# Optimization experiments

Measured on AMD Instinct MI355X. Metric: run time of the kernel, lower is better.

## Reference

```python
import jax, jax.numpy as jnp
import numpy as np

EMBED_DIM = 768
NUM_HEADS = 12
HEAD_DIM = EMBED_DIM // NUM_HEADS


def setup_inputs() -> dict:
    key = jax.random.key(0)
    ks = jax.random.split(key, 9)
    d = EMBED_DIM
    s = 1.0 / np.sqrt(d)
    x = jax.random.normal(ks[0], (1, 4096, d), dtype=jnp.float32)
    # nn.Linear weights stored as [out, in]; init ~ U(-1/sqrt(in), 1/sqrt(in))
    wq = jax.random.uniform(ks[1], (d, d), jnp.float32, -s, s)
    bq = jax.random.uniform(ks[2], (d,), jnp.float32, -s, s)
    wk = jax.random.uniform(ks[3], (d, d), jnp.float32, -s, s)
    bk = jax.random.uniform(ks[4], (d,), jnp.float32, -s, s)
    wv = jax.random.uniform(ks[5], (d, d), jnp.float32, -s, s)
    bv = jax.random.uniform(ks[6], (d,), jnp.float32, -s, s)
    ww = jax.random.uniform(ks[7], (d, d), jnp.float32, -s, s)
    bw = jax.random.uniform(ks[8], (d,), jnp.float32, -s, s)
    return {"x": x, "wq": wq, "bq": bq, "wk": wk, "bk": bk,
            "wv": wv, "bv": bv, "ww": ww, "bw": bw}


def reference(x, wq, bq, wk, bk, wv, bv, ww, bw):
    B, S, D = x.shape
    H, Hd = NUM_HEADS, HEAD_DIM
    # Linear: x @ W^T + b, then split heads -> [B, H, S, Hd]
    def proj(w, b):
        y = x @ w.T + b
        return y.reshape(B, S, H, Hd).transpose(0, 2, 1, 3)
    q = proj(wq, bq)
    k = proj(wk, bk)
    v = proj(wv, bv)
    scores = jnp.einsum('bhqd,bhkd->bhqk', q, k) / jnp.sqrt(jnp.float32(Hd))
    attn = jax.nn.softmax(scores, axis=-1)
    out = jnp.einsum('bhqk,bhkd->bhqd', attn, v)  # [B,H,S,Hd]
    out = out.transpose(0, 2, 1, 3).reshape(B, S, D)
    return out @ ww.T + bw
```

## Files before the change

kernel.cpp:

```cpp
#include <hip/hip_runtime.h>
#include <cstdio>


using u16 = unsigned short;
typedef __bf16 bf16x8 __attribute__((ext_vector_type(8)));
typedef float f32x4 __attribute__((ext_vector_type(4)));
typedef float f32x16 __attribute__((ext_vector_type(16)));
typedef unsigned int u32x4 __attribute__((ext_vector_type(4)));
typedef u16 u16x4 __attribute__((ext_vector_type(4)));

constexpr int SEQ = 4096;
constexpr int DIM = 768;
constexpr int NH = 12;
constexpr int HD = 64;
constexpr int LDT = 72;
constexpr int LDA2 = 40;
constexpr int LDM = 68;
constexpr float SM_PRE = 0.18033688011112042f;
constexpr float DEFER_THR = 8.0f;

__device__ __forceinline__ u16 f2bf(float f) {
  union { float f; unsigned u; } v{f};
  unsigned r = v.u + 0x7fffu + ((v.u >> 16) & 1u);
  return (u16)(r >> 16);
}
__device__ __forceinline__ unsigned cvtpk_bf16(float a, float b) {
  unsigned r;
  asm("v_cvt_pk_bf16_f32 %0, %1, %2" : "=v"(r) : "v"(a), "v"(b));
  return r;
}
__device__ __forceinline__ void swap32(unsigned& a, unsigned& b) {
  asm volatile("v_permlane32_swap_b32 %0, %1" : "+v"(a), "+v"(b));
}
__device__ __forceinline__ bf16x8 bc16(const u16* p) {
  return __builtin_bit_cast(bf16x8, *(const u32x4*)p);
}
__device__ __forceinline__ float fmax3(float a, float b, float c) {
  return fmaxf(fmaxf(a, b), c);
}

__global__ __launch_bounds__(256) void prep_all(const float* __restrict__ x,
                                                const float* __restrict__ wq,
                                                const float* __restrict__ wk,
                                                const float* __restrict__ wv,
                                                u16* __restrict__ xb,
                                                u16* __restrict__ wqb,
                                                u16* __restrict__ wkb,
                                                u16* __restrict__ wvb) {
  constexpr size_t NX = (size_t)SEQ * DIM, NW = (size_t)DIM * DIM;
  size_t i = ((size_t)blockIdx.x * 256 + threadIdx.x) * 8;
  const float* src;
  u16* dst;
  size_t off;
  if (i < NX) { src = x; dst = xb; off = i; }
  else if (i < NX + NW) { src = wq; dst = wqb; off = i - NX; }
  else if (i < NX + 2 * NW) { src = wk; dst = wkb; off = i - NX - 2 * NW + NW; }
  else { src = wv; dst = wvb; off = i - NX - 3 * NW + NW; }
  float4 f0 = *(const float4*)(src + off);
  float4 f1 = *(const float4*)(src + off + 4);
  u32x4 w = {cvtpk_bf16(f0.x, f0.y), cvtpk_bf16(f0.z, f0.w),
             cvtpk_bf16(f1.x, f1.y), cvtpk_bf16(f1.z, f1.w)};
  *(u32x4*)(dst + off) = w;
}

__global__ __launch_bounds__(256) void prep_one(const float* __restrict__ w,
                                                u16* __restrict__ wb) {
  size_t off = ((size_t)blockIdx.x * 256 + threadIdx.x) * 8;
  float4 f0 = *(const float4*)(w + off);
  float4 f1 = *(const float4*)(w + off + 4);
  u32x4 v = {cvtpk_bf16(f0.x, f0.y), cvtpk_bf16(f0.z, f0.w),
             cvtpk_bf16(f1.x, f1.y), cvtpk_bf16(f1.z, f1.w)};
  *(u32x4*)(wb + off) = v;
}

__global__ __launch_bounds__(256) void qkv_gemm(const u16* __restrict__ xb,
                                                const u16* __restrict__ wqb,
                                                const u16* __restrict__ wkb,
                                                const u16* __restrict__ wvb,
                                                const float* __restrict__ bq,
                                                const float* __restrict__ bk,
                                                const float* __restrict__ bv,
                                                u16* __restrict__ Qb,
                                                u16* __restrict__ Kb,
                                                u16* __restrict__ Vtb) {
  __shared__ alignas(16) u16 As[2][64 * LDA2];
  __shared__ alignas(16) u16 Bq[2][64 * LDA2];
  __shared__ alignas(16) u16 Bk[2][64 * LDA2];
  __shared__ alignas(16) u16 Bv[2][64 * LDA2];

  const int tid = threadIdx.x, lane = tid & 63, wave = tid >> 6;
  const int lg = lane >> 4, ln = lane & 15;
  const int bid = blockIdx.x;
  const int swz = (bid & 7) * 96 + (bid >> 3);
  const int mt = swz / 12, nt = swz % 12;
  const int m0 = mt * 64, n0 = nt * 64;
  const int srow = tid >> 2, scol = (tid & 3) * 8;

  f32x4 acc[4][3] = {};

  u32x4 pA, pQ, pK, pV;
  auto pf = [&](int kk) {
    pA = *(const u32x4*)(xb + (size_t)(m0 + srow) * DIM + kk + scol);
    pQ = *(const u32x4*)(wqb + (size_t)(n0 + srow) * DIM + kk + scol);
    pK = *(const u32x4*)(wkb + (size_t)(n0 + srow) * DIM + kk + scol);
    pV = *(const u32x4*)(wvb + (size_t)(n0 + srow) * DIM + kk + scol);
  };
  auto stage = [&](int b) {
    *(u32x4*)&As[b][srow * LDA2 + scol] = pA;
    *(u32x4*)&Bq[b][srow * LDA2 + scol] = pQ;
    *(u32x4*)&Bk[b][srow * LDA2 + scol] = pK;
    *(u32x4*)&Bv[b][srow * LDA2 + scol] = pV;
  };

  constexpr int NS = DIM / 32;
  pf(0);
  stage(0);
  pf(32);
  __syncthreads();

  for (int s = 0; s < NS; ++s) {
    const int cur = s & 1;
    bf16x8 a[4];
#pragma unroll
    for (int i = 0; i < 4; ++i)
      a[i] = bc16(&As[cur][(i * 16 + ln) * LDA2 + lg * 8]);
    bf16x8 fq = bc16(&Bq[cur][(wave * 16 + ln) * LDA2 + lg * 8]);
    bf16x8 fk = bc16(&Bk[cur][(wave * 16 + ln) * LDA2 + lg * 8]);
    bf16x8 fv = bc16(&Bv[cur][(wave * 16 + ln) * LDA2 + lg * 8]);
    if (s + 1 < NS) {
      stage(cur ^ 1);
      if (s + 2 < NS) pf((s + 2) * 32);
    }
#pragma unroll
    for (int i = 0; i < 4; ++i) {
      acc[i][0] = __builtin_amdgcn_mfma_f32_16x16x32_bf16(a[i], fq, acc[i][0], 0, 0, 0);
      acc[i][1] = __builtin_amdgcn_mfma_f32_16x16x32_bf16(a[i], fk, acc[i][1], 0, 0, 0);
      acc[i][2] = __builtin_amdgcn_mfma_f32_16x16x32_bf16(a[i], fv, acc[i][2], 0, 0, 0);
    }
    __syncthreads();
  }

  const int col = n0 + wave * 16 + ln;
  const float bvq = bq[col], bvk = bk[col], bvv = bv[col];
#pragma unroll
  for (int i = 0; i < 4; ++i) {
    const int rowb = m0 + i * 16 + lg * 4;
#pragma unroll
    for (int r = 0; r < 4; ++r) {
      Qb[(size_t)(rowb + r) * DIM + col] = f2bf((acc[i][0][r] + bvq) * SM_PRE);
      Kb[(size_t)(rowb + r) * DIM + col] = f2bf(acc[i][1][r] + bvk);
    }
    u16x4 pk;
#pragma unroll
    for (int r = 0; r < 4; ++r) pk[r] = f2bf(acc[i][2][r] + bvv);
    *(u16x4*)&Vtb[(size_t)col * SEQ + rowb] = pk;
  }
}

__global__ __launch_bounds__(256) void out_gemm(const u16* __restrict__ Ab,
                                                const u16* __restrict__ Wb,
                                                const float* __restrict__ bias,
                                                float* __restrict__ out) {
  __shared__ alignas(16) u16 As[2][64 * LDA2];
  __shared__ alignas(16) u16 Bs[2][64 * LDA2];

  const int tid = threadIdx.x, lane = tid & 63, wave = tid >> 6;
  const int lg = lane >> 4, ln = lane & 15;
  const int bid = blockIdx.x;
  const int swz = (bid & 7) * 96 + (bid >> 3);
  const int mt = swz / 12, nt = swz % 12;
  const int m0 = mt * 64, n0 = nt * 64;
  const int srow = tid >> 2, scol = (tid & 3) * 8;

  f32x4 acc[4] = {};

  u32x4 pA, pB;
  auto pf = [&](int kk) {
    pA = *(const u32x4*)(Ab + (size_t)(m0 + srow) * DIM + kk + scol);
    pB = *(const u32x4*)(Wb + (size_t)(n0 + srow) * DIM + kk + scol);
  };
  auto stage = [&](int b) {
    *(u32x4*)&As[b][srow * LDA2 + scol] = pA;
    *(u32x4*)&Bs[b][srow * LDA2 + scol] = pB;
  };

  constexpr int NS = DIM / 32;
  pf(0);
  stage(0);
  pf(32);
  __syncthreads();

  for (int s = 0; s < NS; ++s) {
    const int cur = s & 1;
    bf16x8 b = bc16(&Bs[cur][(wave * 16 + ln) * LDA2 + lg * 8]);
    bf16x8 a[4];
#pragma unroll
    for (int j = 0; j < 4; ++j)
      a[j] = bc16(&As[cur][(j * 16 + ln) * LDA2 + lg * 8]);
    if (s + 1 < NS) {
      stage(cur ^ 1);
      if (s + 2 < NS) pf((s + 2) * 32);
    }
#pragma unroll
    for (int j = 0; j < 4; ++j)
      acc[j] = __builtin_amdgcn_mfma_f32_16x16x32_bf16(a[j], b, acc[j], 0, 0, 0);
    __syncthreads();
  }

  const int col = n0 + wave * 16 + ln;
  const float bv = bias[col];
#pragma unroll
  for (int j = 0; j < 4; ++j) {
    const int rowb = m0 + j * 16 + lg * 4;
#pragma unroll
    for (int r = 0; r < 4; ++r) out[(size_t)(rowb + r) * DIM + col] = acc[j][r] + bv;
  }
}

__global__ __launch_bounds__(256, 3) void attn_kernel(const u16* __restrict__ Q,
                                                      const u16* __restrict__ K,
                                                      const u16* __restrict__ Vt,
                                                      u16* __restrict__ AO) {
  __shared__ alignas(16) u16 Ks[2][64 * LDT];
  __shared__ alignas(16) u16 Vs[2][64 * LDT];
  __shared__ float sm[4][32], sl[4][32];

  const int tid = threadIdx.x, lane = tid & 63, wave = tid >> 6;
  const int l31 = lane & 31, hi = lane >> 5;
  const int g = wave >> 1, p = wave & 1;
  const int bid = blockIdx.x;
  const int swz = (bid & 7) * 96 + (bid >> 3);
  const int h = swz >> 6;
  const int q0 = (swz & 63) * 64;
  const int qw = q0 + g * 32;

  bf16x8 qf[4];
#pragma unroll
  for (int c = 0; c < 4; ++c)
    qf[c] = bc16(Q + (size_t)(qw + l31) * DIM + h * HD + c * 16 + hi * 8);

  float m_ = -1e30f, l_ = 0.f;
  f32x16 oacc[2] = {};

  const int srow = tid >> 2;
  const int scol = (tid & 3) * 16;

  const u16* Kh = K + (size_t)h * HD;
  const u16* Vh = Vt + (size_t)h * HD * SEQ;
  constexpr int NT = SEQ / 64;

  u32x4 kp0, kp1, vp0, vp1;
  auto pf = [&](int t) {
    const u32x4* s = (const u32x4*)(Kh + (size_t)(t * 64 + srow) * DIM + scol);
    kp0 = s[0]; kp1 = s[1];
    const u32x4* v = (const u32x4*)(Vh + (size_t)srow * SEQ + t * 64 + scol);
    vp0 = v[0]; vp1 = v[1];
  };
  auto stage = [&](int buf) {
    u16* kd = &Ks[buf][srow * LDT + scol];
    *(u32x4*)kd = kp0; *(u32x4*)(kd + 8) = kp1;
    u16* vd = &Vs[buf][srow * LDT + scol];
    *(u32x4*)vd = vp0; *(u32x4*)(vd + 8) = vp1;
  };

  pf(0);
  stage(0);
  pf(1);
  __syncthreads();

  auto round = [&](int t, int cur) {
    bf16x8 kf0 = bc16(&Ks[cur][(p * 32 + l31) * LDT + 0 * 16 + hi * 8]);
    bf16x8 kf1 = bc16(&Ks[cur][(p * 32 + l31) * LDT + 1 * 16 + hi * 8]);
    bf16x8 kf2 = bc16(&Ks[cur][(p * 32 + l31) * LDT + 2 * 16 + hi * 8]);
    bf16x8 kf3 = bc16(&Ks[cur][(p * 32 + l31) * LDT + 3 * 16 + hi * 8]);
    const int vr0 = (0 * 32 + l31) * LDT + p * 32;
    const int vr1 = (1 * 32 + l31) * LDT + p * 32;
    bf16x8 vf00 = bc16(&Vs[cur][vr0 + hi * 8]);
    bf16x8 vf01 = bc16(&Vs[cur][vr0 + 16 + hi * 8]);
    bf16x8 vf10 = bc16(&Vs[cur][vr1 + hi * 8]);
    bf16x8 vf11 = bc16(&Vs[cur][vr1 + 16 + hi * 8]);

    if (t + 1 < NT) {
      stage(cur ^ 1);
      pf(t + 2 < NT ? t + 2 : t + 1);
    }

    f32x16 st = {};
    __builtin_amdgcn_s_setprio(1);
    st = __builtin_amdgcn_mfma_f32_32x32x16_bf16(kf0, qf[0], st, 0, 0, 0);
    st = __builtin_amdgcn_mfma_f32_32x32x16_bf16(kf1, qf[1], st, 0, 0, 0);
    st = __builtin_amdgcn_mfma_f32_32x32x16_bf16(kf2, qf[2], st, 0, 0, 0);
    st = __builtin_amdgcn_mfma_f32_32x32x16_bf16(kf3, qf[3], st, 0, 0, 0);
    __builtin_amdgcn_s_setprio(0);

    float g0 = fmax3(st[0], st[4], st[8]);
    float g1 = fmax3(st[12], st[1], st[5]);
    float g2 = fmax3(st[9], st[13], st[2]);
    float g3 = fmax3(st[6], st[10], st[14]);
    float g4 = fmax3(st[3], st[7], st[11]);
    float pm = fmaxf(fmax3(g0, g1, g2), fmax3(g3, g4, st[15]));
    pm = fmaxf(pm, __shfl_xor(pm, 32));

    if (__ballot(pm > m_ + DEFER_THR)) {
      const float mn = fmaxf(m_, pm);
      const float scl = __builtin_amdgcn_exp2f(m_ - mn);
      l_ *= scl;
      m_ = mn;
      float fac[16];
#pragma unroll
      for (int r = 0; r < 16; ++r)
        fac[r] = __shfl(scl, (r & 3) + 8 * (r >> 2) + 4 * hi);
#pragma unroll
      for (int nd = 0; nd < 2; ++nd)
#pragma unroll
        for (int r = 0; r < 16; ++r) oacc[nd][r] *= fac[r];
    }

#pragma unroll
    for (int r = 0; r < 16; ++r) st[r] = __builtin_amdgcn_exp2f(st[r] - m_);
    {
      float s0 = (st[0] + st[4]) + (st[8] + st[12]);
      float s1 = (st[1] + st[5]) + (st[9] + st[13]);
      float s2 = (st[2] + st[6]) + (st[10] + st[14]);
      float s3 = (st[3] + st[7]) + (st[11] + st[15]);
      float rs = (s0 + s1) + (s2 + s3);
      rs += __shfl_xor(rs, 32);
      l_ += rs;
    }

    unsigned c0 = cvtpk_bf16(st[0], st[1]), c1 = cvtpk_bf16(st[2], st[3]);
    unsigned c2 = cvtpk_bf16(st[4], st[5]), c3 = cvtpk_bf16(st[6], st[7]);
    unsigned c4 = cvtpk_bf16(st[8], st[9]), c5 = cvtpk_bf16(st[10], st[11]);
    unsigned c6 = cvtpk_bf16(st[12], st[13]), c7 = cvtpk_bf16(st[14], st[15]);
    swap32(c0, c2); swap32(c1, c3); swap32(c4, c6); swap32(c5, c7);
    bf16x8 pa0 = __builtin_bit_cast(bf16x8, u32x4{c0, c1, c2, c3});
    bf16x8 pa1 = __builtin_bit_cast(bf16x8, u32x4{c4, c5, c6, c7});

    __builtin_amdgcn_s_setprio(1);
    oacc[0] = __builtin_amdgcn_mfma_f32_32x32x16_bf16(pa0, vf00, oacc[0], 0, 0, 0);
    oacc[0] = __builtin_amdgcn_mfma_f32_32x32x16_bf16(pa1, vf01, oacc[0], 0, 0, 0);
    oacc[1] = __builtin_amdgcn_mfma_f32_32x32x16_bf16(pa0, vf10, oacc[1], 0, 0, 0);
    oacc[1] = __builtin_amdgcn_mfma_f32_32x32x16_bf16(pa1, vf11, oacc[1], 0, 0, 0);
    __builtin_amdgcn_s_setprio(0);
    __syncthreads();
  };

  for (int t = 0; t < NT; t += 2) {
    round(t, 0);
    round(t + 1, 1);
  }

  if (hi == 0) { sm[wave][l31] = m_; sl[wave][l31] = l_; }
  __syncthreads();

  const float m0s = sm[g * 2][l31], m1s = sm[g * 2 + 1][l31];
  const float l0s = sl[g * 2][l31], l1s = sl[g * 2 + 1][l31];
  const float M = fmaxf(m0s, m1s);
  const float L = l0s * __builtin_amdgcn_exp2f(m0s - M) +
                  l1s * __builtin_amdgcn_exp2f(m1s - M);
  const float fac = __builtin_amdgcn_exp2f(m_ - M);
  const float Linv = 1.f / L;
  float facr[16], Lr[16];
#pragma unroll
  for (int r = 0; r < 16; ++r) {
    const int ri = (r & 3) + 8 * (r >> 2) + 4 * hi;
    facr[r] = __shfl(fac, ri);
    Lr[r] = __shfl(Linv, ri);
  }

  float* Om = (float*)Ks;
  if (p == 1) {
#pragma unroll
    for (int nd = 0; nd < 2; ++nd)
#pragma unroll
      for (int r = 0; r < 16; ++r) {
        const int row = (r & 3) + 8 * (r >> 2) + 4 * hi;
        Om[(g * 32 + row) * LDM + nd * 32 + l31] = oacc[nd][r] * facr[r];
      }
  }
  __syncthreads();
  if (p == 0) {
#pragma unroll
    for (int nd = 0; nd < 2; ++nd)
#pragma unroll
      for (int r = 0; r < 16; ++r) {
        const int row = (r & 3) + 8 * (r >> 2) + 4 * hi;
        const float v = (oacc[nd][r] * facr[r] +
                         Om[(g * 32 + row) * LDM + nd * 32 + l31]) * Lr[r];
        AO[(size_t)(qw + row) * DIM + h * HD + nd * 32 + l31] = f2bf(v);
      }
  }
}

extern "C" void kernel_launch(void* const* d_in, const int* in_sizes, int n_in,
                              void* d_out, int out_size, void* d_ws, size_t ws_size,
                              hipStream_t stream) {
  const float* x = (const float*)d_in[0];
  const float* wq = (const float*)d_in[1];
  const float* bq = (const float*)d_in[2];
  const float* wk = (const float*)d_in[3];
  const float* bk = (const float*)d_in[4];
  const float* wv = (const float*)d_in[5];
  const float* bv = (const float*)d_in[6];
  const float* ww = (const float*)d_in[7];
  const float* bw = (const float*)d_in[8];

  const size_t mat = (size_t)SEQ * DIM;
  const size_t nw = (size_t)DIM * DIM;
  if (ws_size < 4 * mat * sizeof(u16)) {
    fprintf(stderr, "kernel_launch: ws too small (%zu)\n", ws_size);
    return;
  }
  u16* Qb = (u16*)d_ws;
  u16* Kb = Qb + mat;
  u16* Vtb = Kb + mat;
  u16* AOb = Vtb + mat;
  u16* xb = AOb;
  u16* wqb = (u16*)d_out;
  u16* wkb = wqb + nw;
  u16* wvb = wkb + nw;
  u16* wwb = Kb;

  prep_all<<<dim3(2400), dim3(256), 0, stream>>>(x, wq, wk, wv, xb, wqb, wkb, wvb);
  qkv_gemm<<<dim3(768), dim3(256), 0, stream>>>(xb, wqb, wkb, wvb, bq, bk, bv, Qb, Kb, Vtb);
  attn_kernel<<<dim3(768), dim3(256), 0, stream>>>(Qb, Kb, Vtb, AOb);
  prep_one<<<dim3(288), dim3(256), 0, stream>>>(ww, wwb);
  out_gemm<<<dim3(768), dim3(256), 0, stream>>>(AOb, wwb, bw, (float*)d_out);
}
```

Baseline: 131.5 us.

## Software-pipeline attention QK and PV MFMAs; fold Ww bf16 conversion into out_gemm

The attention loop is restructured so each iteration's PV MFMAs, which use the previous tile's softmax probabilities and V fragments, are interleaved with the current tile's QK^T MFMAs. A prologue and an epilogue handle the first and last tiles. This lets the softmax of one tile overlap with matrix work and hides V fragment read latency. Separately, the prep_one kernel launch is removed: out_gemm now loads fp32 Ww and converts it to bf16 during LDS staging, which drops one launch but doubles the global bytes for the weight operand and adds conversion work.

```diff
diff --git a/kernel.cpp b/kernel.cpp
--- a/kernel.cpp
+++ b/kernel.cpp
@@ -63,16 +63,6 @@
   *(u32x4*)(dst + off) = w;
 }
 
-__global__ __launch_bounds__(256) void prep_one(const float* __restrict__ w,
-                                                u16* __restrict__ wb) {
-  size_t off = ((size_t)blockIdx.x * 256 + threadIdx.x) * 8;
-  float4 f0 = *(const float4*)(w + off);
-  float4 f1 = *(const float4*)(w + off + 4);
-  u32x4 v = {cvtpk_bf16(f0.x, f0.y), cvtpk_bf16(f0.z, f0.w),
-             cvtpk_bf16(f1.x, f1.y), cvtpk_bf16(f1.z, f1.w)};
-  *(u32x4*)(wb + off) = v;
-}
-
 __global__ __launch_bounds__(256) void qkv_gemm(const u16* __restrict__ xb,
                                                 const u16* __restrict__ wqb,
                                                 const u16* __restrict__ wkb,
@@ -158,7 +148,7 @@
 }
 
 __global__ __launch_bounds__(256) void out_gemm(const u16* __restrict__ Ab,
-                                                const u16* __restrict__ Wb,
+                                                const float* __restrict__ W,
                                                 const float* __restrict__ bias,
                                                 float* __restrict__ out) {
   __shared__ alignas(16) u16 As[2][64 * LDA2];
@@ -174,14 +164,19 @@
 
   f32x4 acc[4] = {};
 
-  u32x4 pA, pB;
+  u32x4 pA;
+  float4 pB0, pB1;
   auto pf = [&](int kk) {
     pA = *(const u32x4*)(Ab + (size_t)(m0 + srow) * DIM + kk + scol);
-    pB = *(const u32x4*)(Wb + (size_t)(n0 + srow) * DIM + kk + scol);
+    const float* w = W + (size_t)(n0 + srow) * DIM + kk + scol;
+    pB0 = *(const float4*)w;
+    pB1 = *(const float4*)(w + 4);
   };
   auto stage = [&](int b) {
     *(u32x4*)&As[b][srow * LDA2 + scol] = pA;
-    *(u32x4*)&Bs[b][srow * LDA2 + scol] = pB;
+    u32x4 wb = {cvtpk_bf16(pB0.x, pB0.y), cvtpk_bf16(pB0.z, pB0.w),
+                cvtpk_bf16(pB1.x, pB1.y), cvtpk_bf16(pB1.z, pB1.w)};
+    *(u32x4*)&Bs[b][srow * LDA2 + scol] = wb;
   };
 
   constexpr int NS = DIM / 32;
@@ -223,7 +218,7 @@
                                                       u16* __restrict__ AO) {
   __shared__ alignas(16) u16 Ks[2][64 * LDT];
   __shared__ alignas(16) u16 Vs[2][64 * LDT];
-  __shared__ float sm[4][32], sl[4][32];
+  __shared__ float smx[4][32], slx[4][32];
 
   const int tid = threadIdx.x, lane = tid & 63, wave = tid >> 6;
   const int l31 = lane & 31, hi = lane >> 5;
@@ -241,10 +236,10 @@
 
   float m_ = -1e30f, l_ = 0.f;
   f32x16 oacc[2] = {};
+  f32x16 st;
 
   const int srow = tid >> 2;
   const int scol = (tid & 3) * 16;
-
   const u16* Kh = K + (size_t)h * HD;
   const u16* Vh = Vt + (size_t)h * HD * SEQ;
   constexpr int NT = SEQ / 64;
@@ -262,37 +257,23 @@
     u16* vd = &Vs[buf][srow * LDT + scol];
     *(u32x4*)vd = vp0; *(u32x4*)(vd + 8) = vp1;
   };
-
-  pf(0);
-  stage(0);
-  pf(1);
-  __syncthreads();
-
-  auto round = [&](int t, int cur) {
-    bf16x8 kf0 = bc16(&Ks[cur][(p * 32 + l31) * LDT + 0 * 16 + hi * 8]);
-    bf16x8 kf1 = bc16(&Ks[cur][(p * 32 + l31) * LDT + 1 * 16 + hi * 8]);
-    bf16x8 kf2 = bc16(&Ks[cur][(p * 32 + l31) * LDT + 2 * 16 + hi * 8]);
-    bf16x8 kf3 = bc16(&Ks[cur][(p * 32 + l31) * LDT + 3 * 16 + hi * 8]);
-    const int vr0 = (0 * 32 + l31) * LDT + p * 32;
-    const int vr1 = (1 * 32 + l31) * LDT + p * 32;
-    bf16x8 vf00 = bc16(&Vs[cur][vr0 + hi * 8]);
-    bf16x8 vf01 = bc16(&Vs[cur][vr0 + 16 + hi * 8]);
-    bf16x8 vf10 = bc16(&Vs[cur][vr1 + hi * 8]);
-    bf16x8 vf11 = bc16(&Vs[cur][vr1 + 16 + hi * 8]);
-
-    if (t + 1 < NT) {
-      stage(cur ^ 1);
-      pf(t + 2 < NT ? t + 2 : t + 1);
-    }
-
-    f32x16 st = {};
-    __builtin_amdgcn_s_setprio(1);
-    st = __builtin_amdgcn_mfma_f32_32x32x16_bf16(kf0, qf[0], st, 0, 0, 0);
-    st = __builtin_amdgcn_mfma_f32_32x32x16_bf16(kf1, qf[1], st, 0, 0, 0);
-    st = __builtin_amdgcn_mfma_f32_32x32x16_bf16(kf2, qf[2], st, 0, 0, 0);
-    st = __builtin_amdgcn_mfma_f32_32x32x16_bf16(kf3, qf[3], st, 0, 0, 0);
-    __builtin_amdgcn_s_setprio(0);
-
+  auto readK = [&](const u16* Kbuf, bf16x8* kf) {
+    const int kr = (p * 32 + l31) * LDT + hi * 8;
+    kf[0] = bc16(&Kbuf[kr]);
+    kf[1] = bc16(&Kbuf[kr + 16]);
+    kf[2] = bc16(&Kbuf[kr + 32]);
+    kf[3] = bc16(&Kbuf[kr + 48]);
+  };
+  auto readV = [&](const u16* Vbuf, bf16x8* vf) {
+    const int vr0 = l31 * LDT + p * 32 + hi * 8;
+    const int vr1 = (32 + l31) * LDT + p * 32 + hi * 8;
+    vf[0] = bc16(&Vbuf[vr0]);
+    vf[1] = bc16(&Vbuf[vr0 + 16]);
+    vf[2] = bc16(&Vbuf[vr1]);
+    vf[3] = bc16(&Vbuf[vr1 + 16]);
+  };
+
+  auto softmax_pa = [&](bf16x8& pa0, bf16x8& pa1) {
     float g0 = fmax3(st[0], st[4], st[8]);
     float g1 = fmax3(st[12], st[1], st[5]);
     float g2 = fmax3(st[9], st[13], st[2]);
@@ -300,7 +281,6 @@
     float g4 = fmax3(st[3], st[7], st[11]);
     float pm = fmaxf(fmax3(g0, g1, g2), fmax3(g3, g4, st[15]));
     pm = fmaxf(pm, __shfl_xor(pm, 32));
-
     if (__ballot(pm > m_ + DEFER_THR)) {
       const float mn = fmaxf(m_, pm);
       const float scl = __builtin_amdgcn_exp2f(m_ - mn);
@@ -311,11 +291,8 @@
       for (int r = 0; r < 16; ++r)
         fac[r] = __shfl(scl, (r & 3) + 8 * (r >> 2) + 4 * hi);
 #pragma unroll
-      for (int nd = 0; nd < 2; ++nd)
-#pragma unroll
-        for (int r = 0; r < 16; ++r) oacc[nd][r] *= fac[r];
-    }
-
+      for (int r = 0; r < 16; ++r) { oacc[0][r] *= fac[r]; oacc[1][r] *= fac[r]; }
+    }
 #pragma unroll
     for (int r = 0; r < 16; ++r) st[r] = __builtin_amdgcn_exp2f(st[r] - m_);
     {
@@ -327,34 +304,81 @@
       rs += __shfl_xor(rs, 32);
       l_ += rs;
     }
-
     unsigned c0 = cvtpk_bf16(st[0], st[1]), c1 = cvtpk_bf16(st[2], st[3]);
     unsigned c2 = cvtpk_bf16(st[4], st[5]), c3 = cvtpk_bf16(st[6], st[7]);
     unsigned c4 = cvtpk_bf16(st[8], st[9]), c5 = cvtpk_bf16(st[10], st[11]);
     unsigned c6 = cvtpk_bf16(st[12], st[13]), c7 = cvtpk_bf16(st[14], st[15]);
     swap32(c0, c2); swap32(c1, c3); swap32(c4, c6); swap32(c5, c7);
-    bf16x8 pa0 = __builtin_bit_cast(bf16x8, u32x4{c0, c1, c2, c3});
-    bf16x8 pa1 = __builtin_bit_cast(bf16x8, u32x4{c4, c5, c6, c7});
-
+    pa0 = __builtin_bit_cast(bf16x8, u32x4{c0, c1, c2, c3});
+    pa1 = __builtin_bit_cast(bf16x8, u32x4{c4, c5, c6, c7});
+  };
+
+  auto body = [&](int t, int cur, bf16x8* vfPrev, bf16x8* vfCur) {
+    bf16x8 kf[4];
+    readK(Ks[cur], kf);
+    if (t + 1 < NT) {
+      stage(cur ^ 1);
+      pf(t + 2 < NT ? t + 2 : t + 1);
+    }
+    bf16x8 pa0, pa1;
+    softmax_pa(pa0, pa1);
     __builtin_amdgcn_s_setprio(1);
-    oacc[0] = __builtin_amdgcn_mfma_f32_32x32x16_bf16(pa0, vf00, oacc[0], 0, 0, 0);
-    oacc[0] = __builtin_amdgcn_mfma_f32_32x32x16_bf16(pa1, vf01, oacc[0], 0, 0, 0);
-    oacc[1] = __builtin_amdgcn_mfma_f32_32x32x16_bf16(pa0, vf10, oacc[1], 0, 0, 0);
-    oacc[1] = __builtin_amdgcn_mfma_f32_32x32x16_bf16(pa1, vf11, oacc[1], 0, 0, 0);
+    st = {};
+    oacc[0] = __builtin_amdgcn_mfma_f32_32x32x16_bf16(pa0, vfPrev[0], oacc[0], 0, 0, 0);
+    st = __builtin_amdgcn_mfma_f32_32x32x16_bf16(kf[0], qf[0], st, 0, 0, 0);
+    oacc[0] = __builtin_amdgcn_mfma_f32_32x32x16_bf16(pa1, vfPrev[1], oacc[0], 0, 0, 0);
+    st = __builtin_amdgcn_mfma_f32_32x32x16_bf16(kf[1], qf[1], st, 0, 0, 0);
+    oacc[1] = __builtin_amdgcn_mfma_f32_32x32x16_bf16(pa0, vfPrev[2], oacc[1], 0, 0, 0);
+    st = __builtin_amdgcn_mfma_f32_32x32x16_bf16(kf[2], qf[2], st, 0, 0, 0);
+    oacc[1] = __builtin_amdgcn_mfma_f32_32x32x16_bf16(pa1, vfPrev[3], oacc[1], 0, 0, 0);
+    st = __builtin_amdgcn_mfma_f32_32x32x16_bf16(kf[3], qf[3], st, 0, 0, 0);
     __builtin_amdgcn_s_setprio(0);
+    readV(Vs[cur], vfCur);
     __syncthreads();
   };
 
-  for (int t = 0; t < NT; t += 2) {
-    round(t, 0);
-    round(t + 1, 1);
-  }
-
-  if (hi == 0) { sm[wave][l31] = m_; sl[wave][l31] = l_; }
+  pf(0);
+  stage(0);
+  pf(1);
   __syncthreads();
 
-  const float m0s = sm[g * 2][l31], m1s = sm[g * 2 + 1][l31];
-  const float l0s = sl[g * 2][l31], l1s = sl[g * 2 + 1][l31];
+  bf16x8 vfA[4], vfB[4];
+  {
+    bf16x8 kf[4];
+    readK(Ks[0], kf);
+    stage(1);
+    pf(2);
+    __builtin_amdgcn_s_setprio(1);
+    st = {};
+    st = __builtin_amdgcn_mfma_f32_32x32x16_bf16(kf[0], qf[0], st, 0, 0, 0);
+    st = __builtin_amdgcn_mfma_f32_32x32x16_bf16(kf[1], qf[1], st, 0, 0, 0);
+    st = __builtin_amdgcn_mfma_f32_32x32x16_bf16(kf[2], qf[2], st, 0, 0, 0);
+    st = __builtin_amdgcn_mfma_f32_32x32x16_bf16(kf[3], qf[3], st, 0, 0, 0);
+    __builtin_amdgcn_s_setprio(0);
+    readV(Vs[0], vfA);
+    __syncthreads();
+  }
+
+  for (int t = 1; t + 1 < NT; t += 2) {
+    body(t, 1, vfA, vfB);
+    body(t + 1, 0, vfB, vfA);
+  }
+  body(NT - 1, 1, vfA, vfB);
+
+  {
+    bf16x8 pa0, pa1;
+    softmax_pa(pa0, pa1);
+    oacc[0] = __builtin_amdgcn_mfma_f32_32x32x16_bf16(pa0, vfB[0], oacc[0], 0, 0, 0);
+    oacc[0] = __builtin_amdgcn_mfma_f32_32x32x16_bf16(pa1, vfB[1], oacc[0], 0, 0, 0);
+    oacc[1] = __builtin_amdgcn_mfma_f32_32x32x16_bf16(pa0, vfB[2], oacc[1], 0, 0, 0);
+    oacc[1] = __builtin_amdgcn_mfma_f32_32x32x16_bf16(pa1, vfB[3], oacc[1], 0, 0, 0);
+  }
+
+  if (hi == 0) { smx[wave][l31] = m_; slx[wave][l31] = l_; }
+  __syncthreads();
+
+  const float m0s = smx[g * 2][l31], m1s = smx[g * 2 + 1][l31];
+  const float l0s = slx[g * 2][l31], l1s = slx[g * 2 + 1][l31];
   const float M = fmaxf(m0s, m1s);
   const float L = l0s * __builtin_amdgcn_exp2f(m0s - M) +
                   l1s * __builtin_amdgcn_exp2f(m1s - M);
@@ -419,11 +443,9 @@
   u16* wqb = (u16*)d_out;
   u16* wkb = wqb + nw;
   u16* wvb = wkb + nw;
-  u16* wwb = Kb;
 
   prep_all<<<dim3(2400), dim3(256), 0, stream>>>(x, wq, wk, wv, xb, wqb, wkb, wvb);
   qkv_gemm<<<dim3(768), dim3(256), 0, stream>>>(xb, wqb, wkb, wvb, bq, bk, bv, Qb, Kb, Vtb);
   attn_kernel<<<dim3(768), dim3(256), 0, stream>>>(Qb, Kb, Vtb, AOb);
-  prep_one<<<dim3(288), dim3(256), 0, stream>>>(ww, wwb);
-  out_gemm<<<dim3(768), dim3(256), 0, stream>>>(AOb, wwb, bw, (float*)d_out);
-}
+  out_gemm<<<dim3(768), dim3(256), 0, stream>>>(AOb, ww, bw, (float*)d_out);
+}
```

New measurement: 135.2 us. +2.9%, slower.
